# Performance work log

Measured on AMD Instinct MI355X. Metric: run time of the kernel, lower is better.

The kernel has to match this reference:

```python
import jax, jax.numpy as jnp
import numpy as np

B, L, H, M = 8, 512, 768, 383
N = M + 1  # +1 dummy epsilon mention
NEG = -10000.0


def _lin(x, W, b):
    return x @ W.T + b


def setup_inputs() -> dict:
    key = jax.random.key(0)
    ks = jax.random.split(key, 26)
    s = 0.02
    inp = {}
    inp["sequence_output"] = jax.random.normal(ks[0], (B, L, H), jnp.float32)
    inp["speaker_emb"] = jax.random.normal(ks[1], (400, H), jnp.float32) * s
    inp["dummy_emb"] = jax.random.normal(ks[2], (1, H), jnp.float32) * s
    inp["W_pair1"] = jax.random.normal(ks[3], (H, 2 * H), jnp.float32) * s
    inp["b_pair1"] = jnp.zeros((H,), jnp.float32)
    inp["W_pair2"] = jax.random.normal(ks[4], (H // 2, H), jnp.float32) * s
    inp["b_pair2"] = jnp.zeros((H // 2,), jnp.float32)
    inp["W_pair3"] = jax.random.normal(ks[5], (1, H // 2), jnp.float32) * s
    inp["b_pair3"] = jnp.zeros((1,), jnp.float32)
    inp["W_m1"] = jax.random.normal(ks[6], (H // 2, H), jnp.float32) * s
    inp["b_m1"] = jnp.zeros((H // 2,), jnp.float32)
    inp["W_m2"] = jax.random.normal(ks[7], (H // 4, H // 2), jnp.float32) * s
    inp["b_m2"] = jnp.zeros((H // 4,), jnp.float32)
    inp["W_m3"] = jax.random.normal(ks[8], (1, H // 4), jnp.float32) * s
    inp["b_m3"] = jnp.zeros((1,), jnp.float32)
    inp["W_c1"] = jax.random.normal(ks[9], (H // 2, H), jnp.float32) * s
    inp["b_c1"] = jnp.zeros((H // 2,), jnp.float32)
    inp["W_c2"] = jax.random.normal(ks[10], (18, H // 2), jnp.float32) * s
    inp["b_c2"] = jnp.zeros((18,), jnp.float32)
    inp["mentions_seg"] = jax.random.randint(ks[11], (M,), 0, B, jnp.int32)
    inp["mention_start"] = jax.random.randint(ks[12], (M,), 0, L, jnp.int32)
    inp["mention_end"] = jax.random.randint(ks[13], (M,), 0, L, jnp.int32)
    inp["speaker_ids"] = jax.random.randint(ks[14], (B, L), 0, 400, jnp.int32)
    second = jnp.arange(1, N, dtype=jnp.int32)  # each real mention is a 'second' exactly once
    first = jax.random.randint(ks[15], (M,), 0, N, jnp.int32) % second  # antecedent strictly before
    inp["link_first"] = first
    inp["link_second"] = second
    inp["character_label"] = jax.random.randint(ks[16], (M,), 0, 18, jnp.int32)
    return inp


def reference(sequence_output, speaker_emb, dummy_emb,
              W_pair1, b_pair1, W_pair2, b_pair2, W_pair3, b_pair3,
              W_m1, b_m1, W_m2, b_m2, W_m3, b_m3,
              W_c1, b_c1, W_c2, b_c2,
              mentions_seg, mention_start, mention_end, speaker_ids,
              link_first, link_second, character_label):
    relu = jax.nn.relu
    # gather mention boundary + speaker reps: [M, H]
    start_rep = sequence_output[mentions_seg, mention_start]
    end_rep = sequence_output[mentions_seg, mention_end]
    spk_rep = speaker_emb[speaker_ids[mentions_seg, mention_start]]
    mention_reps = start_rep + end_rep + spk_rep
    # character linking head: [M, 18]
    char_logits = _lin(relu(_lin(mention_reps, W_c1, b_c1)), W_c2, b_c2)
    # prepend dummy epsilon mention: [N, H]
    all_reps = jnp.concatenate([dummy_emb, mention_reps], axis=0)
    # pairwise MLP; pair[i, j] = MLP(cat(rep_j, rep_i)). Split W_pair1 to avoid [N,N,2H] concat.
    Wa, Wb = W_pair1[:, :H], W_pair1[:, H:]
    A = all_reps @ Wa.T  # contribution of 'first' (column j)
    Bm = all_reps @ Wb.T  # contribution of 'second' (row i)
    h1 = relu(A[None, :, :] + Bm[:, None, :] + b_pair1)  # [N, N, H]
    h2 = relu(jnp.einsum('ijk,hk->ijh', h1, W_pair2) + b_pair2)  # [N, N, H/2]
    pair_scores = jnp.einsum('ijh,oh->ij', h2, W_pair3) + b_pair3[0]  # [N, N]
    # unary mention score: [N]
    ms = (_lin(relu(_lin(relu(_lin(all_reps, W_m1, b_m1)), W_m2, b_m2)), W_m3, b_m3))[:, 0]
    mask = jnp.triu(jnp.ones((N, N), jnp.float32), k=0) * NEG
    mention_scores = pair_scores + ms[None, :] + ms[:, None] + mask
    # linking loss via row-softmax and link gathers
    sm = jax.nn.softmax(mention_scores, axis=1)
    lik = sm[link_second, link_first]  # [num_links]
    col_sum = jnp.zeros((N,), sm.dtype).at[link_second].add(lik)
    nll = -jnp.sum(jnp.log(col_sum[1:]))
    # character cross-entropy (sum reduction)
    logp = jax.nn.log_softmax(char_logits, axis=1)
    ce = -jnp.sum(jnp.take_along_axis(logp, character_label[:, None], axis=1))
    return nll + ce


if __name__ == '__main__':
    out = reference(**setup_inputs())
    print(out)
```

## Files before the change

kernel.cpp:

```cpp
#include <hip/hip_runtime.h>

typedef __bf16 bf16x8 __attribute__((ext_vector_type(8)));
typedef float f32x4 __attribute__((ext_vector_type(4)));

#define WS_ALLREPS 0
#define WS_APRIME  294912
#define WS_BMAT    589824
#define WS_RELUM1  884736
#define WS_RELUC1  1032192
#define WS_MS      1179648
#define WS_SSUM    1180032
#define WS_PF      1180416
#define WS_W2BF    1180800

__device__ __forceinline__ bf16x8 cvt8(float4 a, float4 b) {
  bf16x8 v;
  v[0]=(__bf16)a.x; v[1]=(__bf16)a.y; v[2]=(__bf16)a.z; v[3]=(__bf16)a.w;
  v[4]=(__bf16)b.x; v[5]=(__bf16)b.y; v[6]=(__bf16)b.z; v[7]=(__bf16)b.w;
  return v;
}

__global__ __launch_bounds__(256) void k_build(
    const float* __restrict__ seq, const float* __restrict__ spk_emb,
    const float* __restrict__ dummy, const float* __restrict__ W2,
    const int* __restrict__ seg, const int* __restrict__ mstart,
    const int* __restrict__ mend, const int* __restrict__ spk_ids,
    float* __restrict__ all_reps, __bf16* __restrict__ W2bf) {
  int r = blockIdx.x, t = threadIdx.x;
  if (r < 384) {
    if (r == 0) {
      #pragma unroll
      for (int e = 0; e < 3; ++e) { int k = t + 256*e; all_reps[k] = dummy[k]; }
    } else {
      int m = r - 1;
      int sg = seg[m], st = mstart[m], en = mend[m];
      int sp = spk_ids[sg*512 + st];
      const float* p1 = seq + (size_t)(sg*512 + st)*768;
      const float* p2 = seq + (size_t)(sg*512 + en)*768;
      const float* p3 = spk_emb + (size_t)sp*768;
      #pragma unroll
      for (int e = 0; e < 3; ++e) { int k = t + 256*e; all_reps[r*768+k] = p1[k]+p2[k]+p3[k]; }
    }
  } else {
    int h = r - 384;
    #pragma unroll
    for (int e = 0; e < 3; ++e) { int k = t + 256*e; W2bf[h*768+k] = (__bf16)W2[h*768+k]; }
  }
}

__global__ __launch_bounds__(256) void k_gemmB(
    const float* __restrict__ reps, const float* __restrict__ W1,
    const float* __restrict__ Wm1, const float* __restrict__ Wc1,
    const float* __restrict__ b1, const float* __restrict__ bm1, const float* __restrict__ bc1,
    float* __restrict__ Aprime, float* __restrict__ Bmat,
    float* __restrict__ relu_m1, float* __restrict__ relu_c1) {
  __shared__ bf16x8 lA[128*4];
  __shared__ bf16x8 lB[128*4];
  int nt = blockIdx.x;
  int m0 = blockIdx.y * 128;
  int t = threadIdx.x;
  const float* src; int stride, coloff;
  if (nt < 6)       { src = W1  + (size_t)(nt*128)*1536;      stride = 1536; coloff = 0;   }
  else if (nt < 12) { src = W1  + (size_t)((nt-6)*128)*1536;  stride = 1536; coloff = 768; }
  else if (nt < 15) { src = Wm1 + (size_t)((nt-12)*128)*768;  stride = 768;  coloff = 0;   }
  else              { src = Wc1 + (size_t)((nt-15)*128)*768;  stride = 768;  coloff = 0;   }

  int w = t>>6, l = t&63;
  int wm = w&1, wn = w>>1;
  int lr = l&15, lg = l>>4;

  int r2 = t>>1, half = t&1;
  const float* pa_base = reps + (size_t)(m0+r2)*768 + half*16;
  const float* pb_base = src + (size_t)r2*stride + coloff + half*16;
  int c0 = half*2, c1 = half*2+1;
  int idxA0 = r2*4 + (c0 ^ (r2&3));
  int idxA1 = r2*4 + (c1 ^ (r2&3));

  f32x4 acc[4][4] = {};

  for (int ks = 0; ks < 24; ++ks) {
    int k0 = ks*32;
    {
      float4 f0 = *(const float4*)(pa_base + k0);
      float4 f1 = *(const float4*)(pa_base + k0 + 4);
      float4 f2 = *(const float4*)(pa_base + k0 + 8);
      float4 f3 = *(const float4*)(pa_base + k0 + 12);
      lA[idxA0] = cvt8(f0, f1);
      lA[idxA1] = cvt8(f2, f3);
      float4 g0 = *(const float4*)(pb_base + k0);
      float4 g1 = *(const float4*)(pb_base + k0 + 4);
      float4 g2 = *(const float4*)(pb_base + k0 + 8);
      float4 g3 = *(const float4*)(pb_base + k0 + 12);
      lB[idxA0] = cvt8(g0, g1);
      lB[idxA1] = cvt8(g2, g3);
    }
    __syncthreads();
    bf16x8 af[4], bfr[4];
    #pragma unroll
    for (int fa = 0; fa < 4; ++fa) { int row = wm*64 + fa*16 + lr; af[fa] = lA[row*4 + (lg ^ (row&3))]; }
    #pragma unroll
    for (int fb = 0; fb < 4; ++fb) { int row = wn*64 + fb*16 + lr; bfr[fb] = lB[row*4 + (lg ^ (row&3))]; }
    #pragma unroll
    for (int fa = 0; fa < 4; ++fa)
      #pragma unroll
      for (int fb = 0; fb < 4; ++fb)
        acc[fa][fb] = __builtin_amdgcn_mfma_f32_16x16x32_bf16(af[fa], bfr[fb], acc[fa][fb], 0, 0, 0);
    __syncthreads();
  }

  #pragma unroll
  for (int fa = 0; fa < 4; ++fa) {
    #pragma unroll
    for (int fb = 0; fb < 4; ++fb) {
      #pragma unroll
      for (int reg = 0; reg < 4; ++reg) {
        int m = m0 + wm*64 + fa*16 + lg*4 + reg;
        int nl = wn*64 + fb*16 + lr;
        float v = acc[fa][fb][reg];
        if (nt < 6)       { int n = nt*128 + nl;      Aprime[m*768+n]  = v + b1[n]; }
        else if (nt < 12) { int n = (nt-6)*128 + nl;  Bmat[m*768+n]    = v; }
        else if (nt < 15) { int n = (nt-12)*128 + nl; relu_m1[m*384+n] = fmaxf(v + bm1[n], 0.f); }
        else              { int n = (nt-15)*128 + nl; relu_c1[m*384+n] = fmaxf(v + bc1[n], 0.f); }
      }
    }
  }
}

__global__ __launch_bounds__(192) void k_ms(
    const float* __restrict__ relu_m1, const float* __restrict__ Wm2,
    const float* __restrict__ bm2, const float* __restrict__ Wm3,
    const float* __restrict__ bm3, float* __restrict__ ms) {
  __shared__ float x[384];
  __shared__ float part[3];
  int r = blockIdx.x, t = threadIdx.x;
  x[t] = relu_m1[r*384 + t];
  x[t+192] = relu_m1[r*384 + t + 192];
  __syncthreads();
  float d = 0.f;
  const float4* wv = (const float4*)(Wm2 + (size_t)t*384);
  const float4* xv = (const float4*)x;
  for (int k = 0; k < 96; ++k) {
    float4 a = xv[k], b = wv[k];
    d += a.x*b.x + a.y*b.y + a.z*b.z + a.w*b.w;
  }
  float c = fmaxf(d + bm2[t], 0.f) * Wm3[t];
  c += __shfl_xor(c, 1);  c += __shfl_xor(c, 2);  c += __shfl_xor(c, 4);
  c += __shfl_xor(c, 8);  c += __shfl_xor(c, 16); c += __shfl_xor(c, 32);
  if ((t&63) == 0) part[t>>6] = c;
  __syncthreads();
  if (t == 0) ms[r] = part[0] + part[1] + part[2] + bm3[0];
}

__global__ __launch_bounds__(512) void k_pair(
    const float* __restrict__ Aprime, const float* __restrict__ Bmat,
    const __bf16* __restrict__ W2bf, const float* __restrict__ b2,
    const float* __restrict__ w3, const float* __restrict__ b3,
    const float* __restrict__ ms, const int* __restrict__ lfirst,
    float* __restrict__ Ssum, float* __restrict__ Pf) {
  int jb = blockIdx.x, ib = blockIdx.y;
  if (jb > 2*ib + 1) return;
  __shared__ bf16x8 lA[128*4];
  __shared__ bf16x8 lB[384*4];
  __shared__ float score_lds[128][4];

  int t = threadIdx.x;
  int w = t>>6, l = t&63;
  int wp = w&1, wh = w>>1;
  int lr = l&15, lg = l>>4;
  int i0 = ib*16, j0 = jb*8;

  int p = t>>2, q = t&3;
  const float* pArow = Aprime + (size_t)(j0 + (p&7))*768 + q*8;
  const float* pBrow = Bmat   + (size_t)(i0 + (p>>3))*768 + q*8;
  int idxH = p*4 + (q ^ (p&3));
  const __bf16* pW0 = W2bf + (size_t)p*768       + q*8;
  const __bf16* pW1 = W2bf + (size_t)(p+128)*768 + q*8;
  const __bf16* pW2p = W2bf + (size_t)(p+256)*768 + q*8;
  int idxW0 = p*4       + (q ^ (p&3));
  int idxW1 = (p+128)*4 + (q ^ (p&3));
  int idxW2 = (p+256)*4 + (q ^ (p&3));

  float4 ga0 = *(const float4*)(pArow);
  float4 ga1 = *(const float4*)(pArow + 4);
  float4 gb0 = *(const float4*)(pBrow);
  float4 gb1 = *(const float4*)(pBrow + 4);
  bf16x8 gw0 = *(const bf16x8*)(pW0);
  bf16x8 gw1 = *(const bf16x8*)(pW1);
  bf16x8 gw2 = *(const bf16x8*)(pW2p);

  f32x4 acc[4][6] = {};

  for (int ks = 0; ks < 24; ++ks) {
    {
      float4 r0, r1;
      r0.x = fmaxf(ga0.x + gb0.x, 0.f); r0.y = fmaxf(ga0.y + gb0.y, 0.f);
      r0.z = fmaxf(ga0.z + gb0.z, 0.f); r0.w = fmaxf(ga0.w + gb0.w, 0.f);
      r1.x = fmaxf(ga1.x + gb1.x, 0.f); r1.y = fmaxf(ga1.y + gb1.y, 0.f);
      r1.z = fmaxf(ga1.z + gb1.z, 0.f); r1.w = fmaxf(ga1.w + gb1.w, 0.f);
      lA[idxH] = cvt8(r0, r1);
      lB[idxW0] = gw0; lB[idxW1] = gw1; lB[idxW2] = gw2;
    }
    __syncthreads();
    if (ks < 23) {
      int k0 = (ks+1)*32;
      ga0 = *(const float4*)(pArow + k0);
      ga1 = *(const float4*)(pArow + k0 + 4);
      gb0 = *(const float4*)(pBrow + k0);
      gb1 = *(const float4*)(pBrow + k0 + 4);
      gw0 = *(const bf16x8*)(pW0 + k0);
      gw1 = *(const bf16x8*)(pW1 + k0);
      gw2 = *(const bf16x8*)(pW2p + k0);
    }
    bf16x8 af[4], bfr[6];
    #pragma unroll
    for (int fp = 0; fp < 4; ++fp) { int row = wp*64 + fp*16 + lr; af[fp] = lA[row*4 + (lg ^ (row&3))]; }
    #pragma unroll
    for (int fh = 0; fh < 6; ++fh) { int row = wh*96 + fh*16 + lr; bfr[fh] = lB[row*4 + (lg ^ (row&3))]; }
    #pragma unroll
    for (int fp = 0; fp < 4; ++fp)
      #pragma unroll
      for (int fh = 0; fh < 6; ++fh)
        acc[fp][fh] = __builtin_amdgcn_mfma_f32_16x16x32_bf16(af[fp], bfr[fh], acc[fp][fh], 0, 0, 0);
    __syncthreads();
  }

  float sacc[4][4] = {};
  #pragma unroll
  for (int fh = 0; fh < 6; ++fh) {
    int hcol = wh*96 + fh*16 + lr;
    float bb = b2[hcol], ww = w3[hcol];
    #pragma unroll
    for (int fp = 0; fp < 4; ++fp)
      #pragma unroll
      for (int reg = 0; reg < 4; ++reg)
        sacc[fp][reg] += fmaxf(acc[fp][fh][reg] + bb, 0.f) * ww;
  }
  #pragma unroll
  for (int fp = 0; fp < 4; ++fp) {
    #pragma unroll
    for (int reg = 0; reg < 4; ++reg) {
      float v = sacc[fp][reg];
      v += __shfl_xor(v, 1); v += __shfl_xor(v, 2);
      v += __shfl_xor(v, 4); v += __shfl_xor(v, 8);
      if (lr == 0) score_lds[wp*64 + fp*16 + lg*4 + reg][wh] = v;
    }
  }
  __syncthreads();

  if (t < 128) {
    int pp = t;
    float s = score_lds[pp][0] + score_lds[pp][1] + score_lds[pp][2] + score_lds[pp][3] + b3[0];
    int i = i0 + (pp>>3), j = j0 + (pp&7);
    float e = 0.f;
    if (j < i) {
      float sm = s + ms[j];
      e = __expf(sm);
      if (j == lfirst[i-1]) Pf[i] = sm;
    }
    e += __shfl_xor(e, 1); e += __shfl_xor(e, 2); e += __shfl_xor(e, 4);
    if ((t&7) == 0) atomicAdd(&Ssum[i], e);
  }
}

__global__ __launch_bounds__(64) void k_ce(
    const float* __restrict__ relu_c1, const float* __restrict__ Wc2,
    const float* __restrict__ bc2, const int* __restrict__ label,
    float* __restrict__ out) {
  __shared__ float lg[18];
  int m = blockIdx.x, t = threadIdx.x;
  if (t < 18) {
    const float4* xv = (const float4*)(relu_c1 + (size_t)(m+1)*384);
    const float4* wv = (const float4*)(Wc2 + (size_t)t*384);
    float d = 0.f;
    for (int k = 0; k < 96; ++k) {
      float4 a = xv[k], b = wv[k];
      d += a.x*b.x + a.y*b.y + a.z*b.z + a.w*b.w;
    }
    lg[t] = d + bc2[t];
  }
  __syncthreads();
  if (t == 0) {
    float sum = 0.f;
    for (int c = 0; c < 18; ++c) sum += __expf(lg[c]);
    atomicAdd(out, __logf(sum) - lg[label[m]]);
  }
}

__global__ __launch_bounds__(384) void k_nll(
    const float* __restrict__ Ssum, const float* __restrict__ Pf,
    float* __restrict__ out) {
  int i = threadIdx.x;
  if (i >= 1) atomicAdd(out, __logf(Ssum[i]) - Pf[i]);
}

extern "C" void kernel_launch(void* const* d_in, const int* in_sizes, int n_in,
                              void* d_out, int out_size, void* d_ws, size_t ws_size,
                              hipStream_t stream) {
  (void)in_sizes; (void)n_in; (void)out_size; (void)ws_size;
  const float* seq   = (const float*)d_in[0];
  const float* spk   = (const float*)d_in[1];
  const float* dummy = (const float*)d_in[2];
  const float* W1    = (const float*)d_in[3];
  const float* b1    = (const float*)d_in[4];
  const float* W2    = (const float*)d_in[5];
  const float* b2    = (const float*)d_in[6];
  const float* W3    = (const float*)d_in[7];
  const float* b3    = (const float*)d_in[8];
  const float* Wm1   = (const float*)d_in[9];
  const float* bm1   = (const float*)d_in[10];
  const float* Wm2   = (const float*)d_in[11];
  const float* bm2   = (const float*)d_in[12];
  const float* Wm3   = (const float*)d_in[13];
  const float* bm3   = (const float*)d_in[14];
  const float* Wc1   = (const float*)d_in[15];
  const float* bc1   = (const float*)d_in[16];
  const float* Wc2   = (const float*)d_in[17];
  const float* bc2   = (const float*)d_in[18];
  const int* seg     = (const int*)d_in[19];
  const int* mstart  = (const int*)d_in[20];
  const int* mend    = (const int*)d_in[21];
  const int* spk_ids = (const int*)d_in[22];
  const int* lfirst  = (const int*)d_in[23];
  const int* clabel  = (const int*)d_in[25];

  float* ws = (float*)d_ws;
  float* all_reps = ws + WS_ALLREPS;
  float* Aprime   = ws + WS_APRIME;
  float* Bmat     = ws + WS_BMAT;
  float* relu_m1  = ws + WS_RELUM1;
  float* relu_c1  = ws + WS_RELUC1;
  float* msv      = ws + WS_MS;
  float* Ssum     = ws + WS_SSUM;
  float* Pf       = ws + WS_PF;
  __bf16* W2bf    = (__bf16*)(ws + WS_W2BF);
  float* out      = (float*)d_out;

  hipMemsetAsync(out, 0, sizeof(float), stream);
  hipMemsetAsync(Ssum, 0, 384*sizeof(float), stream);

  k_build<<<768, 256, 0, stream>>>(seq, spk, dummy, W2, seg, mstart, mend, spk_ids, all_reps, W2bf);
  k_gemmB<<<dim3(18,3), 256, 0, stream>>>(all_reps, W1, Wm1, Wc1, b1, bm1, bc1, Aprime, Bmat, relu_m1, relu_c1);
  k_ms<<<384, 192, 0, stream>>>(relu_m1, Wm2, bm2, Wm3, bm3, msv);
  k_pair<<<dim3(48,24), 512, 0, stream>>>(Aprime, Bmat, W2bf, b2, W3, b3, msv, lfirst, Ssum, Pf);
  k_ce<<<383, 64, 0, stream>>>(relu_c1, Wc2, bc2, clabel, out);
  k_nll<<<1, 384, 0, stream>>>(Ssum, Pf, out);
}
```

Measured before the change: 281.8 us.

## Double-buffer pair GEMM LDS, compact triangular grid, retile gemmB and batch ms rows

The pair kernel now uses double-buffered LDS with one barrier per k-step, raises wave priority around the MFMA block, and maps a flat 1D grid onto the lower-triangular block set, so no blocks launch only to exit. gemmB moves to 64-row tiles, doubling its block count, and the mention-score kernel processes 8 rows per block so each Wm2 load is reused eight times. A new swizzle pattern changes the LDS bank mapping. Together these aim to improve latency hiding and occupancy, at the cost of more LDS per pair block and a sqrt-based index computation.

```diff
diff --git a/kernel.cpp b/kernel.cpp
--- a/kernel.cpp
+++ b/kernel.cpp
@@ -13,6 +13,8 @@
 #define WS_PF      1180416
 #define WS_W2BF    1180800
 
+#define SWZ(row,c) (((row)<<2) + ((c) ^ (((row)>>1)&3)))
+
 __device__ __forceinline__ bf16x8 cvt8(float4 a, float4 b) {
   bf16x8 v;
   v[0]=(__bf16)a.x; v[1]=(__bf16)a.y; v[2]=(__bf16)a.z; v[3]=(__bf16)a.w;
@@ -54,10 +56,10 @@
     const float* __restrict__ b1, const float* __restrict__ bm1, const float* __restrict__ bc1,
     float* __restrict__ Aprime, float* __restrict__ Bmat,
     float* __restrict__ relu_m1, float* __restrict__ relu_c1) {
-  __shared__ bf16x8 lA[128*4];
-  __shared__ bf16x8 lB[128*4];
+  __shared__ bf16x8 lA[256];
+  __shared__ bf16x8 lB[512];
   int nt = blockIdx.x;
-  int m0 = blockIdx.y * 128;
+  int m0 = blockIdx.y * 64;
   int t = threadIdx.x;
   const float* src; int stride, coloff;
   if (nt < 6)       { src = W1  + (size_t)(nt*128)*1536;      stride = 1536; coloff = 0;   }
@@ -69,39 +71,35 @@
   int wm = w&1, wn = w>>1;
   int lr = l&15, lg = l>>4;
 
-  int r2 = t>>1, half = t&1;
-  const float* pa_base = reps + (size_t)(m0+r2)*768 + half*16;
-  const float* pb_base = src + (size_t)r2*stride + coloff + half*16;
-  int c0 = half*2, c1 = half*2+1;
-  int idxA0 = r2*4 + (c0 ^ (r2&3));
-  int idxA1 = r2*4 + (c1 ^ (r2&3));
-
-  f32x4 acc[4][4] = {};
+  int p = t>>2, q = t&3;
+  const float* pa  = reps + (size_t)(m0+p)*768 + q*8;
+  const float* pb0 = src + (size_t)p*stride + coloff + q*8;
+  const float* pb1 = src + (size_t)(p+64)*stride + coloff + q*8;
+  int ia  = SWZ(p, q);
+  int ib0 = SWZ(p, q);
+  int ib1 = SWZ(p+64, q);
+
+  f32x4 acc[2][4] = {};
 
   for (int ks = 0; ks < 24; ++ks) {
     int k0 = ks*32;
-    {
-      float4 f0 = *(const float4*)(pa_base + k0);
-      float4 f1 = *(const float4*)(pa_base + k0 + 4);
-      float4 f2 = *(const float4*)(pa_base + k0 + 8);
-      float4 f3 = *(const float4*)(pa_base + k0 + 12);
-      lA[idxA0] = cvt8(f0, f1);
-      lA[idxA1] = cvt8(f2, f3);
-      float4 g0 = *(const float4*)(pb_base + k0);
-      float4 g1 = *(const float4*)(pb_base + k0 + 4);
-      float4 g2 = *(const float4*)(pb_base + k0 + 8);
-      float4 g3 = *(const float4*)(pb_base + k0 + 12);
-      lB[idxA0] = cvt8(g0, g1);
-      lB[idxA1] = cvt8(g2, g3);
-    }
+    float4 a0 = *(const float4*)(pa + k0);
+    float4 a1 = *(const float4*)(pa + k0 + 4);
+    float4 b0 = *(const float4*)(pb0 + k0);
+    float4 b1v = *(const float4*)(pb0 + k0 + 4);
+    float4 c0 = *(const float4*)(pb1 + k0);
+    float4 c1v = *(const float4*)(pb1 + k0 + 4);
+    lA[ia]  = cvt8(a0, a1);
+    lB[ib0] = cvt8(b0, b1v);
+    lB[ib1] = cvt8(c0, c1v);
     __syncthreads();
-    bf16x8 af[4], bfr[4];
-    #pragma unroll
-    for (int fa = 0; fa < 4; ++fa) { int row = wm*64 + fa*16 + lr; af[fa] = lA[row*4 + (lg ^ (row&3))]; }
-    #pragma unroll
-    for (int fb = 0; fb < 4; ++fb) { int row = wn*64 + fb*16 + lr; bfr[fb] = lB[row*4 + (lg ^ (row&3))]; }
-    #pragma unroll
-    for (int fa = 0; fa < 4; ++fa)
+    bf16x8 af[2], bfr[4];
+    #pragma unroll
+    for (int fa = 0; fa < 2; ++fa) { int row = wm*32 + fa*16 + lr; af[fa] = lA[SWZ(row, lg)]; }
+    #pragma unroll
+    for (int fb = 0; fb < 4; ++fb) { int row = wn*64 + fb*16 + lr; bfr[fb] = lB[SWZ(row, lg)]; }
+    #pragma unroll
+    for (int fa = 0; fa < 2; ++fa)
       #pragma unroll
       for (int fb = 0; fb < 4; ++fb)
         acc[fa][fb] = __builtin_amdgcn_mfma_f32_16x16x32_bf16(af[fa], bfr[fb], acc[fa][fb], 0, 0, 0);
@@ -109,12 +107,12 @@
   }
 
   #pragma unroll
-  for (int fa = 0; fa < 4; ++fa) {
+  for (int fa = 0; fa < 2; ++fa) {
     #pragma unroll
     for (int fb = 0; fb < 4; ++fb) {
       #pragma unroll
       for (int reg = 0; reg < 4; ++reg) {
-        int m = m0 + wm*64 + fa*16 + lg*4 + reg;
+        int m = m0 + wm*32 + fa*16 + lg*4 + reg;
         int nl = wn*64 + fb*16 + lr;
         float v = acc[fa][fb][reg];
         if (nt < 6)       { int n = nt*128 + nl;      Aprime[m*768+n]  = v + b1[n]; }
@@ -130,25 +128,34 @@
     const float* __restrict__ relu_m1, const float* __restrict__ Wm2,
     const float* __restrict__ bm2, const float* __restrict__ Wm3,
     const float* __restrict__ bm3, float* __restrict__ ms) {
-  __shared__ float x[384];
-  __shared__ float part[3];
-  int r = blockIdx.x, t = threadIdx.x;
-  x[t] = relu_m1[r*384 + t];
-  x[t+192] = relu_m1[r*384 + t + 192];
+  __shared__ float x[8][384];
+  __shared__ float part[8][3];
+  int r0 = blockIdx.x*8, t = threadIdx.x;
+  const float4* srcv = (const float4*)(relu_m1 + (size_t)r0*384);
+  float4* dstv = (float4*)&x[0][0];
+  #pragma unroll
+  for (int e = 0; e < 4; ++e) dstv[t + 192*e] = srcv[t + 192*e];
   __syncthreads();
-  float d = 0.f;
+  float a[8] = {};
   const float4* wv = (const float4*)(Wm2 + (size_t)t*384);
-  const float4* xv = (const float4*)x;
   for (int k = 0; k < 96; ++k) {
-    float4 a = xv[k], b = wv[k];
-    d += a.x*b.x + a.y*b.y + a.z*b.z + a.w*b.w;
-  }
-  float c = fmaxf(d + bm2[t], 0.f) * Wm3[t];
-  c += __shfl_xor(c, 1);  c += __shfl_xor(c, 2);  c += __shfl_xor(c, 4);
-  c += __shfl_xor(c, 8);  c += __shfl_xor(c, 16); c += __shfl_xor(c, 32);
-  if ((t&63) == 0) part[t>>6] = c;
+    float4 wq = wv[k];
+    #pragma unroll
+    for (int r = 0; r < 8; ++r) {
+      float4 xq = *(const float4*)&x[r][k*4];
+      a[r] += wq.x*xq.x + wq.y*xq.y + wq.z*xq.z + wq.w*xq.w;
+    }
+  }
+  float wm3 = Wm3[t], bb = bm2[t];
+  #pragma unroll
+  for (int r = 0; r < 8; ++r) {
+    float c = fmaxf(a[r] + bb, 0.f) * wm3;
+    c += __shfl_xor(c, 1);  c += __shfl_xor(c, 2);  c += __shfl_xor(c, 4);
+    c += __shfl_xor(c, 8);  c += __shfl_xor(c, 16); c += __shfl_xor(c, 32);
+    if ((t&63) == 0) part[r][t>>6] = c;
+  }
   __syncthreads();
-  if (t == 0) ms[r] = part[0] + part[1] + part[2] + bm3[0];
+  if (t < 8) ms[r0+t] = part[t][0] + part[t][1] + part[t][2] + bm3[0];
 }
 
 __global__ __launch_bounds__(512) void k_pair(
@@ -157,71 +164,77 @@
     const float* __restrict__ w3, const float* __restrict__ b3,
     const float* __restrict__ ms, const int* __restrict__ lfirst,
     float* __restrict__ Ssum, float* __restrict__ Pf) {
-  int jb = blockIdx.x, ib = blockIdx.y;
-  if (jb > 2*ib + 1) return;
-  __shared__ bf16x8 lA[128*4];
-  __shared__ bf16x8 lB[384*4];
+  int bid = blockIdx.x;
+  int ib = (int)((__fsqrt_rn(4.0f*bid + 1.0f) - 1.0f) * 0.5f);
+  while ((ib+1)*(ib+2) <= bid) ++ib;
+  while (ib*(ib+1) > bid) --ib;
+  int jb = bid - ib*(ib+1);
+  int i0 = ib*16, j0 = jb*8;
+
+  __shared__ bf16x8 lA[2][512];
+  __shared__ bf16x8 lB[2][1536];
   __shared__ float score_lds[128][4];
 
   int t = threadIdx.x;
   int w = t>>6, l = t&63;
   int wp = w&1, wh = w>>1;
   int lr = l&15, lg = l>>4;
-  int i0 = ib*16, j0 = jb*8;
 
   int p = t>>2, q = t&3;
   const float* pArow = Aprime + (size_t)(j0 + (p&7))*768 + q*8;
   const float* pBrow = Bmat   + (size_t)(i0 + (p>>3))*768 + q*8;
-  int idxH = p*4 + (q ^ (p&3));
   const __bf16* pW0 = W2bf + (size_t)p*768       + q*8;
   const __bf16* pW1 = W2bf + (size_t)(p+128)*768 + q*8;
   const __bf16* pW2p = W2bf + (size_t)(p+256)*768 + q*8;
-  int idxW0 = p*4       + (q ^ (p&3));
-  int idxW1 = (p+128)*4 + (q ^ (p&3));
-  int idxW2 = (p+256)*4 + (q ^ (p&3));
-
-  float4 ga0 = *(const float4*)(pArow);
-  float4 ga1 = *(const float4*)(pArow + 4);
-  float4 gb0 = *(const float4*)(pBrow);
-  float4 gb1 = *(const float4*)(pBrow + 4);
-  bf16x8 gw0 = *(const bf16x8*)(pW0);
-  bf16x8 gw1 = *(const bf16x8*)(pW1);
-  bf16x8 gw2 = *(const bf16x8*)(pW2p);
+  int idxH  = SWZ(p, q);
+  int idxW0 = SWZ(p, q);
+  int idxW1 = SWZ(p+128, q);
+  int idxW2 = SWZ(p+256, q);
+
+  float4 ga0, ga1, gb0, gb1;
+  bf16x8 gw0, gw1, gw2;
+
+  #define LOADG(k0) { \
+    ga0 = *(const float4*)(pArow + (k0)); \
+    ga1 = *(const float4*)(pArow + (k0) + 4); \
+    gb0 = *(const float4*)(pBrow + (k0)); \
+    gb1 = *(const float4*)(pBrow + (k0) + 4); \
+    gw0 = *(const bf16x8*)(pW0  + (k0)); \
+    gw1 = *(const bf16x8*)(pW1  + (k0)); \
+    gw2 = *(const bf16x8*)(pW2p + (k0)); }
+
+  #define WRITEB(buf) { \
+    float4 r0, r1; \
+    r0.x = fmaxf(ga0.x + gb0.x, 0.f); r0.y = fmaxf(ga0.y + gb0.y, 0.f); \
+    r0.z = fmaxf(ga0.z + gb0.z, 0.f); r0.w = fmaxf(ga0.w + gb0.w, 0.f); \
+    r1.x = fmaxf(ga1.x + gb1.x, 0.f); r1.y = fmaxf(ga1.y + gb1.y, 0.f); \
+    r1.z = fmaxf(ga1.z + gb1.z, 0.f); r1.w = fmaxf(ga1.w + gb1.w, 0.f); \
+    lA[buf][idxH]  = cvt8(r0, r1); \
+    lB[buf][idxW0] = gw0; lB[buf][idxW1] = gw1; lB[buf][idxW2] = gw2; }
+
+  LOADG(0);
+  WRITEB(0);
 
   f32x4 acc[4][6] = {};
+  int cur = 0;
 
   for (int ks = 0; ks < 24; ++ks) {
-    {
-      float4 r0, r1;
-      r0.x = fmaxf(ga0.x + gb0.x, 0.f); r0.y = fmaxf(ga0.y + gb0.y, 0.f);
-      r0.z = fmaxf(ga0.z + gb0.z, 0.f); r0.w = fmaxf(ga0.w + gb0.w, 0.f);
-      r1.x = fmaxf(ga1.x + gb1.x, 0.f); r1.y = fmaxf(ga1.y + gb1.y, 0.f);
-      r1.z = fmaxf(ga1.z + gb1.z, 0.f); r1.w = fmaxf(ga1.w + gb1.w, 0.f);
-      lA[idxH] = cvt8(r0, r1);
-      lB[idxW0] = gw0; lB[idxW1] = gw1; lB[idxW2] = gw2;
-    }
     __syncthreads();
-    if (ks < 23) {
-      int k0 = (ks+1)*32;
-      ga0 = *(const float4*)(pArow + k0);
-      ga1 = *(const float4*)(pArow + k0 + 4);
-      gb0 = *(const float4*)(pBrow + k0);
-      gb1 = *(const float4*)(pBrow + k0 + 4);
-      gw0 = *(const bf16x8*)(pW0 + k0);
-      gw1 = *(const bf16x8*)(pW1 + k0);
-      gw2 = *(const bf16x8*)(pW2p + k0);
-    }
+    if (ks < 23) LOADG((ks+1)*32);
     bf16x8 af[4], bfr[6];
     #pragma unroll
-    for (int fp = 0; fp < 4; ++fp) { int row = wp*64 + fp*16 + lr; af[fp] = lA[row*4 + (lg ^ (row&3))]; }
-    #pragma unroll
-    for (int fh = 0; fh < 6; ++fh) { int row = wh*96 + fh*16 + lr; bfr[fh] = lB[row*4 + (lg ^ (row&3))]; }
+    for (int fp = 0; fp < 4; ++fp) { int row = wp*64 + fp*16 + lr; af[fp] = lA[cur][SWZ(row, lg)]; }
+    #pragma unroll
+    for (int fh = 0; fh < 6; ++fh) { int row = wh*96 + fh*16 + lr; bfr[fh] = lB[cur][SWZ(row, lg)]; }
+    __builtin_amdgcn_s_setprio(1);
     #pragma unroll
     for (int fp = 0; fp < 4; ++fp)
       #pragma unroll
       for (int fh = 0; fh < 6; ++fh)
         acc[fp][fh] = __builtin_amdgcn_mfma_f32_16x16x32_bf16(af[fp], bfr[fh], acc[fp][fh], 0, 0, 0);
-    __syncthreads();
+    __builtin_amdgcn_s_setprio(0);
+    if (ks < 23) WRITEB(cur^1);
+    cur ^= 1;
   }
 
   float sacc[4][4] = {};
@@ -339,9 +352,9 @@
   hipMemsetAsync(Ssum, 0, 384*sizeof(float), stream);
 
   k_build<<<768, 256, 0, stream>>>(seq, spk, dummy, W2, seg, mstart, mend, spk_ids, all_reps, W2bf);
-  k_gemmB<<<dim3(18,3), 256, 0, stream>>>(all_reps, W1, Wm1, Wc1, b1, bm1, bc1, Aprime, Bmat, relu_m1, relu_c1);
-  k_ms<<<384, 192, 0, stream>>>(relu_m1, Wm2, bm2, Wm3, bm3, msv);
-  k_pair<<<dim3(48,24), 512, 0, stream>>>(Aprime, Bmat, W2bf, b2, W3, b3, msv, lfirst, Ssum, Pf);
+  k_gemmB<<<dim3(18,6), 256, 0, stream>>>(all_reps, W1, Wm1, Wc1, b1, bm1, bc1, Aprime, Bmat, relu_m1, relu_c1);
+  k_ms<<<48, 192, 0, stream>>>(relu_m1, Wm2, bm2, Wm3, bm3, msv);
+  k_pair<<<600, 512, 0, stream>>>(Aprime, Bmat, W2bf, b2, W3, b3, msv, lfirst, Ssum, Pf);
   k_ce<<<383, 64, 0, stream>>>(relu_c1, Wc2, bc2, clabel, out);
   k_nll<<<1, 384, 0, stream>>>(Ssum, Pf, out);
 }
```

After: 261.2 us. 1.08x faster.
